# Kernel tuning notes

Hardware: AMD Instinct MI355X
Metric: run time of the kernel (lower is better)

The kernel has to match this reference:

```python
import jax, jax.numpy as jnp
import numpy as np

B, S, D, H, NL, V, E, DFF = 4, 512, 768, 12, 2, 32000, 8, 3072
CF = 1.25
HD = D // H


def setup_inputs() -> dict:
    key = jax.random.key(0)
    ks = jax.random.split(key, 12)
    r = lambda i, shape: jax.random.normal(ks[i], shape, jnp.float32) * 0.02
    return {
        "src": jax.random.randint(ks[0], (B, S), 0, V),
        "src_pad_mask": jnp.zeros((B, S), bool),
        "emb": r(1, (V, D)),
        "qkv_w": r(2, (NL, 3 * D, D)), "qkv_b": jnp.zeros((NL, 3 * D), jnp.float32),
        "out_w": r(3, (NL, D, D)), "out_b": jnp.zeros((NL, D), jnp.float32),
        "wr": r(4, (NL, D, E)),
        "w1": r(5, (NL, E, D, DFF)), "b1": jnp.zeros((NL, E, DFF), jnp.float32),
        "w2": r(6, (NL, E, DFF, D)), "b2": jnp.zeros((NL, E, D), jnp.float32),
        "ln1_g": jnp.ones((NL, D), jnp.float32), "ln1_b": jnp.zeros((NL, D), jnp.float32),
        "ln2_g": jnp.ones((NL, D), jnp.float32), "ln2_b": jnp.zeros((NL, D), jnp.float32),
        "lnf_g": jnp.ones((D,), jnp.float32), "lnf_b": jnp.zeros((D,), jnp.float32),
    }


def layernorm(x, g, b, eps=1e-5):
    mu = jnp.mean(x, -1, keepdims=True)
    var = jnp.mean((x - mu) ** 2, -1, keepdims=True)
    return (x - mu) * jax.lax.rsqrt(var + eps) * g + b


def pos_encoding():
    pos = jnp.arange(S, dtype=jnp.float32)[:, None]
    i = jnp.arange(0, D, 2, dtype=jnp.float32)
    ang = pos * jnp.exp(-(i / D) * jnp.log(jnp.float32(10000.0)))  # [S, D/2]
    pe = jnp.zeros((S, D), jnp.float32)
    pe = pe.at[:, 0::2].set(jnp.sin(ang)).at[:, 1::2].set(jnp.cos(ang))
    return pe


def mha(x, wqkv, bqkv, wo, bo, pad):
    qkv = x @ wqkv.T + bqkv
    q, k, v = jnp.split(qkv, 3, axis=-1)
    q = q.reshape(B, S, H, HD); k = k.reshape(B, S, H, HD); v = v.reshape(B, S, H, HD)
    sc = jnp.einsum('bqhd,bkhd->bhqk', q, k) * (1.0 / float(HD) ** 0.5)
    sc = jnp.where(pad[:, None, None, :], jnp.float32(-1e9), sc)
    at = jax.nn.softmax(sc, -1)
    o = jnp.einsum('bhqk,bkhd->bqhd', at, v).reshape(B, S, D)
    return o @ wo.T + bo


def switch_ffn(x, token_mask, wr, w1, b1, w2, b2):
    # Switch Transformer top-1 routing with capacity drop.
    T = B * S
    cap = int(CF * T / E)
    xf = x.reshape(T, D)
    vm = token_mask.reshape(T).astype(x.dtype)
    logits = xf @ wr                                   # [T, E]
    probs = jax.nn.softmax(logits, -1)
    idx = jnp.argmax(probs, -1)
    gate = jnp.take_along_axis(probs, idx[:, None], -1)[:, 0]
    oh = jax.nn.one_hot(idx, E, dtype=x.dtype) * vm[:, None]      # [T, E]
    pos = jnp.cumsum(oh, axis=0) * oh                  # 1-indexed position in expert
    keep = ((pos > 0) & (pos <= cap)).astype(x.dtype)
    disp = keep[:, :, None] * jax.nn.one_hot((pos - 1).astype(jnp.int32), cap, dtype=x.dtype)  # [T,E,C]
    comb = disp * gate[:, None, None]
    ein = jnp.einsum('tec,td->ecd', disp, xf)          # [E, C, D]
    hid = jax.nn.relu(jnp.einsum('ecd,edf->ecf', ein, w1) + b1[:, None, :])
    eo = jnp.einsum('ecf,efd->ecd', hid, w2) + b2[:, None, :]
    y = jnp.einsum('tec,ecd->td', comb, eo).reshape(B, S, D)
    denom = jnp.maximum(vm.sum(), 1.0)
    me = (probs * vm[:, None]).sum(0) / denom
    ce = oh.sum(0) / denom
    lb = jnp.float32(E) * jnp.sum(me * ce)
    z = jnp.sum((jax.nn.logsumexp(logits, -1) ** 2) * vm) / denom
    return y, lb, z


def forward(src, src_pad_mask, emb, qkv_w, qkv_b, out_w, out_b, wr, w1, b1, w2, b2,
            ln1_g, ln1_b, ln2_g, ln2_b, lnf_g, lnf_b):
    x = emb[src] * jnp.float32(float(D) ** 0.5) + pos_encoding()[None]
    token_mask = ~src_pad_mask
    lbs, zs = [], []
    for l in range(NL):
        xn = layernorm(x, ln1_g[l], ln1_b[l])
        x = x + mha(xn, qkv_w[l], qkv_b[l], out_w[l], out_b[l], src_pad_mask)
        xn = layernorm(x, ln2_g[l], ln2_b[l])
        y, lb, z = switch_ffn(xn, token_mask, wr[l], w1[l], b1[l], w2[l], b2[l])
        x = x + y
        lbs.append(lb); zs.append(z)
    x = layernorm(x, lnf_g, lnf_b)
    return x, jnp.stack(lbs).mean(), jnp.stack(zs).mean()


def reference(src, src_pad_mask, emb, qkv_w, qkv_b, out_w, out_b, wr, w1, b1, w2, b2,
              ln1_g, ln1_b, ln2_g, ln2_b, lnf_g, lnf_b):
    return forward(src, src_pad_mask, emb, qkv_w, qkv_b, out_w, out_b, wr, w1, b1, w2, b2,
                   ln1_g, ln1_b, ln2_g, ln2_b, lnf_g, lnf_b)
```

## Files before the change

kernel.cpp:

```cpp
#include <hip/hip_runtime.h>

#define BB 4
#define SS 512
#define DD 768
#define HH 12
#define NLAYER 2
#define EE 8
#define DFF 3072
#define TT 2048
#define CAP 320
#define HD 64

typedef unsigned short u16;
typedef long long ll;
typedef _Float16 f16x8 __attribute__((ext_vector_type(8)));
typedef float f32x4 __attribute__((ext_vector_type(4)));

union F16U { _Float16 h; u16 u; };

__device__ __forceinline__ void split2h(float v, u16& h0, u16& h1) {
    F16U c0; c0.h = (_Float16)v;
    float r = (v - (float)c0.h) * 4096.0f;
    F16U c1; c1.h = (_Float16)r;
    h0 = c0.u; h1 = c1.u;
}
__device__ __forceinline__ float rec2h(u16 a, u16 b) {
    F16U c0, c1; c0.u = a; c1.u = b;
    return (float)c0.h + (float)c1.h * (1.0f / 4096.0f);
}

#define MFMA16(a, b, c) __builtin_amdgcn_mfma_f32_16x16x32_f16(a, b, c, 0, 0, 0)

struct GemmP {
    const u16* A = nullptr; ll sAp = 0;
    const void* B = nullptr; ll sBp = 0;
    const float* bias = nullptr; ll biasStride = 0;
    void* C = nullptr; ll sCp = 0;
    int M = 0, N = 0, K = 0, lda = 0, ldb = 0, ldc = 0;
    int modA = 1; ll sA1 = 0, sA2 = 0;
    int modB = 1; ll sB1 = 0, sB2 = 0;
    int modC = 1; ll sC1 = 0, sC2 = 0;
    float alpha = 1.f;
    int flags = 0;
    int KS = 1; ll partStride = 0;
    int Jc = 1;
};

#define PADK 36

template<bool BTRANS, int NS>
__global__ __launch_bounds__(256) void gemm_kernel(GemmP p) {
    __shared__ u16 Al[NS][128][PADK];
    __shared__ u16 Bl[NS][128][PADK];
    const int tid = threadIdx.x;

    int bx, by, bz;
    {
        int gx = gridDim.x, gy = gridDim.y;
        int NBt = gx * gy * gridDim.z;
        int L = blockIdx.x + gx * (blockIdx.y + gy * blockIdx.z);
        int q = NBt >> 3, r = NBt & 7;
        int xcd = L & 7, wi = L >> 3;
        int c = (xcd < r) ? xcd * (q + 1) + wi : r * (q + 1) + (xcd - r) * q + wi;
        int Jc = p.Jc;
        int gxJ = gx * Jc;
        int sj = c / gxJ;
        int t = c - sj * gxJ;
        bx = t / Jc;
        int j = sj * Jc + (t - (t / Jc) * Jc);
        by = j % gy; bz = j / gy;
    }
    const int n0 = bx * 128, m0 = by * 128;
    const int slice = bz % p.KS;
    const int z = bz / p.KS;
    const int kslice = p.K / p.KS;
    const int k0 = slice * kslice;
    const int nkt = kslice >> 5;

    const u16* Ap = p.A + (ll)(z % p.modA) * p.sA1 + (ll)(z / p.modA) * p.sA2 + k0;
    const ll zB = (ll)(z % p.modB) * p.sB1 + (ll)(z / p.modB) * p.sB2;
    const ll zC = (ll)(z % p.modC) * p.sC1 + (ll)(z / p.modC) * p.sC2;
    const u16* Bpu = BTRANS ? ((const u16*)p.B + zB + k0) : nullptr;
    const float* Bpf = BTRANS ? nullptr : ((const float*)p.B + zB);

    const int lane = tid & 63, wid = tid >> 6;
    const int wm = (wid >> 1) * 64, wn = (wid & 1) * 64;
    const int ar = lane & 15, kg = (lane >> 4) * 8;

    f32x4 acc0[4][4] = {};
    f32x4 acc1[4][4] = {};

    uint4 ra[2 * NS];
    uint4 rb[2 * NS];
    float4 rbf4[4];

    auto loadA = [&](int kt) {
        #pragma unroll
        for (int s = 0; s < NS; ++s)
            #pragma unroll
            for (int h = 0; h < 2; ++h) {
                int c = tid + h * 256, row = c >> 2, q = c & 3;
                int gm = m0 + row;
                uint4 v = {0u, 0u, 0u, 0u};
                if (gm < p.M) v = *(const uint4*)(Ap + (ll)s * p.sAp + (size_t)gm * p.lda + kt * 32 + q * 8);
                ra[s * 2 + h] = v;
            }
    };
    auto storeA = [&]() {
        #pragma unroll
        for (int s = 0; s < NS; ++s)
            #pragma unroll
            for (int h = 0; h < 2; ++h) {
                int c = tid + h * 256, row = c >> 2, q = c & 3;
                *(uint4*)&Al[s][row][q * 8] = ra[s * 2 + h];
            }
    };
    auto loadB = [&](int kt) {
        if (BTRANS) {
            #pragma unroll
            for (int s = 0; s < NS; ++s)
                #pragma unroll
                for (int h = 0; h < 2; ++h) {
                    int c = tid + h * 256, row = c >> 2, q = c & 3;
                    int gn = n0 + row;
                    uint4 v = {0u, 0u, 0u, 0u};
                    if (gn < p.N) v = *(const uint4*)(Bpu + (ll)s * p.sBp + (size_t)gn * p.ldb + kt * 32 + q * 8);
                    rb[s * 2 + h] = v;
                }
        } else {
            #pragma unroll
            for (int it = 0; it < 4; ++it) {
                int kk = (tid >> 5) + it * 8;
                int gn = n0 + (tid & 31) * 4;
                float4 v = {0.f, 0.f, 0.f, 0.f};
                if (gn < p.N) v = *(const float4*)(Bpf + (size_t)(k0 + kt * 32 + kk) * p.ldb + gn);
                rbf4[it] = v;
            }
        }
    };
    auto storeB = [&]() {
        if (BTRANS) {
            #pragma unroll
            for (int s = 0; s < NS; ++s)
                #pragma unroll
                for (int h = 0; h < 2; ++h) {
                    int c = tid + h * 256, row = c >> 2, q = c & 3;
                    *(uint4*)&Bl[s][row][q * 8] = rb[s * 2 + h];
                }
        } else {
            int c4 = (tid & 31) * 4;
            #pragma unroll
            for (int it = 0; it < 4; ++it) {
                int kk = (tid >> 5) + it * 8;
                float vv[4] = {rbf4[it].x, rbf4[it].y, rbf4[it].z, rbf4[it].w};
                #pragma unroll
                for (int e = 0; e < 4; ++e) {
                    u16 h0, h1;
                    split2h(vv[e], h0, h1);
                    Bl[0][c4 + e][kk] = h0;
                    if (NS == 2) Bl[1][c4 + e][kk] = h1;
                }
            }
        }
    };

    loadA(0); loadB(0);
    for (int kt = 0; kt < nkt; ++kt) {
        storeA(); storeB();
        __syncthreads();
        if (kt + 1 < nkt) { loadA(kt + 1); loadB(kt + 1); }
        f16x8 b0r[4], b1r[4];
        #pragma unroll
        for (int j = 0; j < 4; ++j) {
            b0r[j] = *(const f16x8*)&Bl[0][wn + j * 16 + ar][kg];
            if (NS == 2) b1r[j] = *(const f16x8*)&Bl[1][wn + j * 16 + ar][kg];
        }
        #pragma unroll
        for (int i = 0; i < 4; ++i) {
            f16x8 a0 = *(const f16x8*)&Al[0][wm + i * 16 + ar][kg];
            f16x8 a1;
            if (NS == 2) a1 = *(const f16x8*)&Al[1][wm + i * 16 + ar][kg];
            #pragma unroll
            for (int j = 0; j < 4; ++j) {
                acc0[i][j] = MFMA16(a0, b0r[j], acc0[i][j]);
                if (NS == 2) {
                    acc1[i][j] = MFMA16(a0, b1r[j], acc1[i][j]);
                    acc1[i][j] = MFMA16(a1, b0r[j], acc1[i][j]);
                }
            }
        }
        __syncthreads();
    }

    const bool doPart = (p.flags & 16);
    float* Cpart = doPart ? ((float*)p.C + (ll)slice * p.partStride + zC) : nullptr;
    const float* biasp = (p.flags & 1) ? (p.bias + (ll)z * p.biasStride) : nullptr;
    u16* C0 = (!doPart && (p.flags & 8)) ? ((u16*)p.C + zC) : nullptr;
    u16* C1 = C0 ? (C0 + p.sCp) : nullptr;
    float* Cf = (!doPart && !(p.flags & 8)) ? ((float*)p.C + zC) : nullptr;
    #pragma unroll
    for (int i = 0; i < 4; ++i) {
        #pragma unroll
        for (int j = 0; j < 4; ++j) {
            int gc = n0 + wn + j * 16 + (lane & 15);
            if (gc >= p.N) continue;
            int gr0 = m0 + wm + i * 16 + (lane >> 4) * 4;
            #pragma unroll
            for (int r = 0; r < 4; ++r) {
                int gr = gr0 + r;
                if (gr >= p.M) continue;
                float v = acc0[i][j][r];
                if (NS == 2) v += acc1[i][j][r] * (1.0f / 4096.0f);
                v *= p.alpha;
                size_t off = (size_t)gr * p.ldc + gc;
                if (doPart) { Cpart[off] = v; continue; }
                if (p.flags & 1) v = __fadd_rn(v, biasp[gc]);
                if (p.flags & 2) v = fmaxf(v, 0.f);
                if (p.flags & 8) { u16 h0, h1; split2h(v, h0, h1); C0[off] = h0; C1[off] = h1; }
                else Cf[off] = v;
            }
        }
    }
}

__global__ __launch_bounds__(256) void flash_kernel(
    const u16* __restrict__ qkvp, ll sQp,
    const u16* __restrict__ vTp, ll sVp,
    const unsigned char* __restrict__ pad,
    u16* __restrict__ attnp, ll sOp) {
    __shared__ u16 KV[2][64][68];
    __shared__ u16 Pl[2][4][16][68];

    int L = blockIdx.x;
    int c = (L & 7) * 48 + (L >> 3);
    int bh = c >> 3, qt = c & 7;
    int b = bh / HH, h = bh % HH;
    int lane = threadIdx.x & 63, wv = threadIdx.x >> 6;
    int qbase = b * SS + qt * 64 + wv * 16;

    int spl = threadIdx.x >> 7;
    int srr = threadIdx.x & 127;
    int srow = srr >> 1, shalf = srr & 1;

    f16x8 qf[2][2];
    {
        const u16* qr = qkvp + (size_t)(qbase + (lane & 15)) * (3 * DD) + h * HD + (lane >> 4) * 8;
        #pragma unroll
        for (int kt2 = 0; kt2 < 2; ++kt2)
            #pragma unroll
            for (int pl = 0; pl < 2; ++pl)
                qf[kt2][pl] = *(const f16x8*)(qr + (ll)pl * sQp + kt2 * 32);
    }

    f32x4 S[32];
    #pragma unroll
    for (int kv = 0; kv < 8; ++kv) {
        const u16* gk = qkvp + (size_t)(b * SS + kv * 64 + srow) * (3 * DD) + DD + h * HD + (ll)spl * sQp;
        #pragma unroll
        for (int qq = 0; qq < 4; ++qq) {
            int off = shalf * 32 + qq * 8;
            *(uint4*)&KV[spl][srow][off] = *(const uint4*)(gk + off);
        }
        __syncthreads();
        #pragma unroll
        for (int nf = 0; nf < 4; ++nf) {
            f32x4 a0 = {}, a1 = {};
            #pragma unroll
            for (int kt2 = 0; kt2 < 2; ++kt2) {
                f16x8 b0 = *(const f16x8*)&KV[0][nf * 16 + (lane & 15)][kt2 * 32 + (lane >> 4) * 8];
                f16x8 b1 = *(const f16x8*)&KV[1][nf * 16 + (lane & 15)][kt2 * 32 + (lane >> 4) * 8];
                a0 = MFMA16(qf[kt2][0], b0, a0);
                a1 = MFMA16(qf[kt2][0], b1, a1);
                a1 = MFMA16(qf[kt2][1], b0, a1);
            }
            int col = kv * 64 + nf * 16 + (lane & 15);
            bool msk = pad[b * SS + col] != 0;
            #pragma unroll
            for (int r = 0; r < 4; ++r) {
                float v = (a0[r] + a1[r] * (1.0f / 4096.0f)) * 0.125f;
                S[kv * 4 + nf][r] = msk ? -1e9f : v;
            }
        }
        __syncthreads();
    }

    float mx[4] = {-1e30f, -1e30f, -1e30f, -1e30f}, sm[4] = {0.f, 0.f, 0.f, 0.f}, inv[4];
    #pragma unroll
    for (int f = 0; f < 32; ++f)
        #pragma unroll
        for (int r = 0; r < 4; ++r) mx[r] = fmaxf(mx[r], S[f][r]);
    #pragma unroll
    for (int r = 0; r < 4; ++r) {
        #pragma unroll
        for (int off = 1; off < 16; off <<= 1) mx[r] = fmaxf(mx[r], __shfl_xor(mx[r], off));
    }
    #pragma unroll
    for (int f = 0; f < 32; ++f)
        #pragma unroll
        for (int r = 0; r < 4; ++r) { float e = expf(S[f][r] - mx[r]); S[f][r] = e; sm[r] += e; }
    #pragma unroll
    for (int r = 0; r < 4; ++r) {
        #pragma unroll
        for (int off = 1; off < 16; off <<= 1) sm[r] += __shfl_xor(sm[r], off);
        inv[r] = 1.f / sm[r];
    }

    f32x4 p0[4] = {}, p1[4] = {};
    #pragma unroll
    for (int kv = 0; kv < 8; ++kv) {
        const u16* gv = vTp + (size_t)bh * HD * SS + (size_t)srow * SS + kv * 64 + (ll)spl * sVp;
        #pragma unroll
        for (int qq = 0; qq < 4; ++qq) {
            int off = shalf * 32 + qq * 8;
            *(uint4*)&KV[spl][srow][off] = *(const uint4*)(gv + off);
        }
        #pragma unroll
        for (int nf = 0; nf < 4; ++nf)
            #pragma unroll
            for (int r = 0; r < 4; ++r) {
                float v = S[kv * 4 + nf][r] * inv[r];
                u16 h0, h1; split2h(v, h0, h1);
                Pl[0][wv][(lane >> 4) * 4 + r][nf * 16 + (lane & 15)] = h0;
                Pl[1][wv][(lane >> 4) * 4 + r][nf * 16 + (lane & 15)] = h1;
            }
        __syncthreads();
        f16x8 pa[2][2];
        #pragma unroll
        for (int kt2 = 0; kt2 < 2; ++kt2)
            #pragma unroll
            for (int pl = 0; pl < 2; ++pl)
                pa[kt2][pl] = *(const f16x8*)&Pl[pl][wv][lane & 15][kt2 * 32 + (lane >> 4) * 8];
        #pragma unroll
        for (int df = 0; df < 4; ++df) {
            #pragma unroll
            for (int kt2 = 0; kt2 < 2; ++kt2) {
                f16x8 v0 = *(const f16x8*)&KV[0][df * 16 + (lane & 15)][kt2 * 32 + (lane >> 4) * 8];
                f16x8 v1 = *(const f16x8*)&KV[1][df * 16 + (lane & 15)][kt2 * 32 + (lane >> 4) * 8];
                p0[df] = MFMA16(pa[kt2][0], v0, p0[df]);
                p1[df] = MFMA16(pa[kt2][0], v1, p1[df]);
                p1[df] = MFMA16(pa[kt2][1], v0, p1[df]);
            }
        }
        __syncthreads();
    }

    #pragma unroll
    for (int df = 0; df < 4; ++df)
        #pragma unroll
        for (int r = 0; r < 4; ++r) {
            float v = p0[df][r] + p1[df][r] * (1.0f / 4096.0f);
            int row = qbase + (lane >> 4) * 4 + r;
            int col = h * HD + df * 16 + (lane & 15);
            u16 h0, h1; split2h(v, h0, h1);
            attnp[(size_t)row * DD + col] = h0;
            attnp[(size_t)row * DD + col + sOp] = h1;
        }
}

struct RedP {
    const float* part = nullptr; ll partStride = 0; int KS = 1;
    float* outf = nullptr;
    u16* o0 = nullptr; ll planeStride = 0;
    const float* bias = nullptr; ll biasStride = 0; ll batchElems = 1; int Nc = 1;
    const float* src = nullptr;
    ll total = 0; int mode = 0;
};
__global__ void reduce_kernel(RedP p) {
    ll e0 = ((ll)blockIdx.x * 256 + threadIdx.x) * 4;
    if (e0 >= p.total) return;
    float4 s = *(const float4*)(p.part + e0);
    for (int k = 1; k < p.KS; ++k) {
        float4 t = *(const float4*)(p.part + (ll)k * p.partStride + e0);
        s.x += t.x; s.y += t.y; s.z += t.z; s.w += t.w;
    }
    if (p.mode & 1) {
        ll b = e0 / p.batchElems;
        int d = (int)(e0 % p.Nc);
        float4 bv = *(const float4*)(p.bias + b * p.biasStride + d);
        s.x = __fadd_rn(s.x, bv.x); s.y = __fadd_rn(s.y, bv.y);
        s.z = __fadd_rn(s.z, bv.z); s.w = __fadd_rn(s.w, bv.w);
    }
    if (p.mode & 4) {
        float4 t = *(const float4*)(p.src + e0);
        s.x = __fadd_rn(s.x, t.x); s.y = __fadd_rn(s.y, t.y);
        s.z = __fadd_rn(s.z, t.z); s.w = __fadd_rn(s.w, t.w);
    }
    if (p.mode & 2) { s.x = fmaxf(s.x, 0.f); s.y = fmaxf(s.y, 0.f); s.z = fmaxf(s.z, 0.f); s.w = fmaxf(s.w, 0.f); }
    if (p.mode & 8) {
        u16 t0[4], t1[4];
        float vv[4] = {s.x, s.y, s.z, s.w};
        #pragma unroll
        for (int e = 0; e < 4; ++e) split2h(vv[e], t0[e], t1[e]);
        *(uint2*)(p.o0 + e0) = *(uint2*)t0;
        *(uint2*)(p.o0 + p.planeStride + e0) = *(uint2*)t1;
    } else {
        *(float4*)(p.outf + e0) = s;
    }
}

__global__ void wsplit_kernel(const float* __restrict__ w, u16* __restrict__ p0,
                              ll planeStride, ll total) {
    ll e0 = ((ll)blockIdx.x * 256 + threadIdx.x) * 4;
    if (e0 >= total) return;
    float4 v = *(const float4*)(w + e0);
    u16 t0[4], t1[4];
    float vv[4] = {v.x, v.y, v.z, v.w};
    #pragma unroll
    for (int e = 0; e < 4; ++e) split2h(vv[e], t0[e], t1[e]);
    *(uint2*)(p0 + e0) = *(uint2*)t0;
    *(uint2*)(p0 + planeStride + e0) = *(uint2*)t1;
}

__global__ void vtrans_kernel(const u16* __restrict__ qkvp, ll sQp,
                              u16* __restrict__ vTp, ll sVp) {
    __shared__ float t[32][33];
    int z = blockIdx.z;
    int b = z / HH, h = z % HH;
    int c0 = blockIdx.x * 32, r0 = blockIdx.y * 32;
    int tx = threadIdx.x, ty = threadIdx.y;
    const u16* in = qkvp + (size_t)(b * SS) * (3 * DD) + 2 * DD + h * HD;
    #pragma unroll
    for (int i = 0; i < 32; i += 8) {
        size_t o = (size_t)(r0 + ty + i) * (3 * DD) + c0 + tx;
        t[ty + i][tx] = rec2h(in[o], in[o + sQp]);
    }
    __syncthreads();
    u16* out = vTp + (size_t)z * HD * SS;
    #pragma unroll
    for (int i = 0; i < 32; i += 8) {
        size_t o = (size_t)(c0 + ty + i) * SS + r0 + tx;
        u16 h0, h1; split2h(t[tx][ty + i], h0, h1);
        out[o] = h0; out[o + sVp] = h1;
    }
}

__global__ void pe_kernel(float* __restrict__ pe) {
    int s = blockIdx.x, tid = threadIdx.x;
    const float lg = 9.210340371976184f;
    #pragma unroll
    for (int j = 0; j < 3; ++j) {
        int d = j * 256 + tid;
        int half = d >> 1;
        float fi = (float)(2 * half) / 768.0f;
        float arg = __fmul_rn(-fi, lg);
        float freq = (float)exp((double)arg);
        float ang = __fmul_rn((float)s, freq);
        double da = (double)ang;
        pe[(size_t)s * DD + d] = (d & 1) ? (float)cos(da) : (float)sin(da);
    }
}

__global__ void embed_kernel(const int* __restrict__ src, const float* __restrict__ emb,
                             const float* __restrict__ pe, float* __restrict__ x) {
    int t = blockIdx.x, tid = threadIdx.x;
    int s = t & (SS - 1);
    int tok = src[t];
    const float sq = 27.712812921102035f;
    #pragma unroll
    for (int j = 0; j < 3; ++j) {
        int d = j * 256 + tid;
        float e = emb[(size_t)tok * DD + d];
        x[(size_t)t * DD + d] = __fadd_rn(__fmul_rn(e, sq), pe[(size_t)s * DD + d]);
    }
}

__global__ void ln_kernel(const float* __restrict__ x, const float* __restrict__ g,
                          const float* __restrict__ b, float* __restrict__ outf,
                          u16* __restrict__ op, ll planeStride) {
    int t = blockIdx.x, tid = threadIdx.x;
    const float* xr = x + (size_t)t * DD;
    float v[3], s = 0.f, sq = 0.f;
    #pragma unroll
    for (int j = 0; j < 3; ++j) { v[j] = xr[tid + j * 256]; s += v[j]; sq += v[j] * v[j]; }
    #pragma unroll
    for (int off = 32; off; off >>= 1) { s += __shfl_xor(s, off); sq += __shfl_xor(sq, off); }
    __shared__ float rs[4], rq[4];
    int wid = tid >> 6;
    if ((tid & 63) == 0) { rs[wid] = s; rq[wid] = sq; }
    __syncthreads();
    s = rs[0] + rs[1] + rs[2] + rs[3];
    sq = rq[0] + rq[1] + rq[2] + rq[3];
    float mu = s / 768.0f;
    float var = sq / 768.0f - mu * mu;
    float rstd = rsqrtf(var + 1e-5f);
    #pragma unroll
    for (int j = 0; j < 3; ++j) {
        int d = tid + j * 256;
        float y = __fadd_rn(__fmul_rn(__fmul_rn(v[j] - mu, rstd), g[d]), b[d]);
        if (outf) outf[(size_t)t * DD + d] = y;
        size_t o = (size_t)t * DD + d;
        u16 h0, h1; split2h(y, h0, h1);
        op[o] = h0; op[o + planeStride] = h1;
    }
}

__global__ void router_kernel(const float* __restrict__ xn, const float* __restrict__ wr,
                              const unsigned char* __restrict__ pad,
                              float* __restrict__ probs, float* __restrict__ lsev,
                              float* __restrict__ gate, int* __restrict__ idx) {
    int t = blockIdx.x, lane = threadIdx.x;
    float a[8] = {0.f, 0.f, 0.f, 0.f, 0.f, 0.f, 0.f, 0.f};
    const float* xr = xn + (size_t)t * DD;
    for (int d = lane; d < DD; d += 64) {
        float xv = xr[d];
        const float* w = wr + (size_t)d * EE;
        #pragma unroll
        for (int e = 0; e < 8; ++e) a[e] += xv * w[e];
    }
    #pragma unroll
    for (int off = 32; off; off >>= 1)
        #pragma unroll
        for (int e = 0; e < 8; ++e) a[e] += __shfl_xor(a[e], off);
    if (lane == 0) {
        int vm = (pad[t] == 0);
        float mx = a[0]; int bi = 0;
        #pragma unroll
        for (int e = 1; e < 8; ++e) if (a[e] > mx) { mx = a[e]; bi = e; }
        float ex[8], sum = 0.f;
        #pragma unroll
        for (int e = 0; e < 8; ++e) { ex[e] = expf(a[e] - mx); sum += ex[e]; }
        float inv = 1.f / sum;
        #pragma unroll
        for (int e = 0; e < 8; ++e) probs[(size_t)t * EE + e] = vm ? ex[e] * inv : 0.f;
        lsev[t] = vm ? (mx + logf(sum)) : 0.f;
        gate[t] = ex[bi] * inv;
        idx[t] = vm ? bi : -1;
    }
}

__global__ void route_scan_kernel(const int* __restrict__ idx, const float* __restrict__ probs,
                                  const float* __restrict__ lsev, int* __restrict__ slot,
                                  int* __restrict__ tos, float* __restrict__ acc) {
    int lane = threadIdx.x;
    int base = lane * 32;
    int ev[32];
    int c[8] = {0, 0, 0, 0, 0, 0, 0, 0};
    #pragma unroll
    for (int i = 0; i < 32; ++i) {
        int e = idx[base + i];
        ev[i] = e;
        #pragma unroll
        for (int q = 0; q < 8; ++q) c[q] += (e == q);
    }
    int excl[8], tot[8];
    #pragma unroll
    for (int e = 0; e < 8; ++e) {
        int v = c[e];
        #pragma unroll
        for (int off = 1; off < 64; off <<= 1) {
            int n = __shfl_up(v, off);
            if (lane >= off) v += n;
        }
        excl[e] = v - c[e];
        tot[e] = __shfl(v, 63);
    }
    int r[8];
    #pragma unroll
    for (int e = 0; e < 8; ++e) r[e] = excl[e];
    #pragma unroll
    for (int i = 0; i < 32; ++i) {
        int t = base + i, e = ev[i], s = -1;
        if (e >= 0) {
            int pos = 0;
            #pragma unroll
            for (int q = 0; q < 8; ++q) if (e == q) { r[q]++; pos = r[q]; }
            if (pos <= CAP) { s = e * CAP + pos - 1; tos[s] = t; }
        }
        slot[t] = s;
    }
    float pa[8] = {0.f, 0.f, 0.f, 0.f, 0.f, 0.f, 0.f, 0.f};
    float l2 = 0.f, vld = 0.f;
    #pragma unroll
    for (int i = 0; i < 32; ++i) {
        int t = base + i;
        float lv = lsev[t];
        l2 += lv * lv;
        if (ev[i] >= 0) vld += 1.f;
        #pragma unroll
        for (int e = 0; e < 8; ++e) pa[e] += probs[(size_t)t * EE + e];
    }
    #pragma unroll
    for (int off = 32; off; off >>= 1) {
        #pragma unroll
        for (int e = 0; e < 8; ++e) pa[e] += __shfl_xor(pa[e], off);
        l2 += __shfl_xor(l2, off);
        vld += __shfl_xor(vld, off);
    }
    if (lane == 0) {
        float denom = fmaxf(vld, 1.f);
        float lb = 0.f;
        #pragma unroll
        for (int e = 0; e < 8; ++e) lb += (pa[e] / denom) * ((float)tot[e] / denom);
        lb *= 8.f;
        acc[0] += lb;
        acc[1] += l2 / denom;
    }
}

__global__ void gather_kernel(const int* __restrict__ tos, const u16* __restrict__ xnp,
                              ll sXp, u16* __restrict__ einp, ll sEp) {
    int s = blockIdx.x;
    int tid = threadIdx.x;
    if (tid >= 192) return;
    int pl = tid / 96, q = tid % 96;
    int t = tos[s];
    uint4 v = {0u, 0u, 0u, 0u};
    if (t >= 0) v = *(const uint4*)(xnp + (ll)pl * sXp + (size_t)t * DD + q * 8);
    *(uint4*)(einp + (ll)pl * sEp + (size_t)s * DD + q * 8) = v;
}

__global__ void combine_kernel(const int* __restrict__ slot, const float* __restrict__ gate,
                               const float* __restrict__ eo, float* __restrict__ x) {
    int t = blockIdx.x, tid = threadIdx.x;
    int s = slot[t];
    if (s < 0) return;
    float gv = gate[t];
    #pragma unroll
    for (int j = 0; j < 3; ++j) {
        int d = j * 256 + tid;
        size_t o = (size_t)t * DD + d;
        x[o] = __fadd_rn(x[o], __fmul_rn(gv, eo[(size_t)s * DD + d]));
    }
}

__global__ void finalize_kernel(const float* __restrict__ acc, float* __restrict__ out) {
    out[(size_t)TT * DD] = acc[0] * (1.f / NLAYER);
    out[(size_t)TT * DD + 1] = acc[1] * (1.f / NLAYER);
}

static inline void run_gemm(bool btrans, int ns, const GemmP& p, dim3 grid, hipStream_t s) {
    if (btrans) {
        gemm_kernel<true, 2><<<grid, 256, 0, s>>>(p);
    } else {
        if (ns == 2) gemm_kernel<false, 2><<<grid, 256, 0, s>>>(p);
        else gemm_kernel<false, 1><<<grid, 256, 0, s>>>(p);
    }
}
static inline void run_reduce(const RedP& r, hipStream_t s) {
    reduce_kernel<<<(int)((r.total / 4 + 255) / 256), 256, 0, s>>>(r);
}

extern "C" void kernel_launch(void* const* d_in, const int* in_sizes, int n_in,
                              void* d_out, int out_size, void* d_ws, size_t ws_size,
                              hipStream_t stream) {
    const int* src = (const int*)d_in[0];
    const unsigned char* pad = (const unsigned char*)d_in[1];
    const float* emb = (const float*)d_in[2];
    const float* qkv_w = (const float*)d_in[3];
    const float* qkv_b = (const float*)d_in[4];
    const float* out_w = (const float*)d_in[5];
    const float* out_b = (const float*)d_in[6];
    const float* wr = (const float*)d_in[7];
    const float* w1 = (const float*)d_in[8];
    const float* b1 = (const float*)d_in[9];
    const float* w2 = (const float*)d_in[10];
    const float* b2 = (const float*)d_in[11];
    const float* ln1_g = (const float*)d_in[12];
    const float* ln1_b = (const float*)d_in[13];
    const float* ln2_g = (const float*)d_in[14];
    const float* ln2_b = (const float*)d_in[15];
    const float* lnf_g = (const float*)d_in[16];
    const float* lnf_b = (const float*)d_in[17];

    char* w = (char*)d_ws;
    size_t off = 0;
    auto alloc = [&](size_t bytes) -> void* {
        void* p = w + off;
        off += (bytes + 255) & ~(size_t)255;
        return p;
    };
    float* x      = (float*)alloc((size_t)TT * DD * 4);
    float* xn     = (float*)alloc((size_t)TT * DD * 4);
    float* peT    = (float*)alloc((size_t)SS * DD * 4);
    u16*   xnp    = (u16*)  alloc((size_t)2 * TT * DD * 2);
    u16*   qkvp   = (u16*)  alloc((size_t)2 * TT * 3 * DD * 2);
    u16*   vTp    = (u16*)  alloc((size_t)2 * BB * HH * HD * SS * 2);
    u16*   attnp  = (u16*)  alloc((size_t)2 * TT * DD * 2);
    u16*   einp   = (u16*)  alloc((size_t)2 * EE * CAP * DD * 2);
    u16*   hidp   = (u16*)  alloc((size_t)2 * EE * CAP * DFF * 2);
    float* eo     = (float*)alloc((size_t)EE * CAP * DD * 4);
    char*  regB   = (char*) alloc((size_t)2 * EE * CAP * DFF * 4);
    u16*   qkvwp  = (u16*)  alloc((size_t)2 * NLAYER * 3 * DD * DD * 2);
    u16*   owp    = (u16*)  alloc((size_t)2 * NLAYER * DD * DD * 2);
    float* probs  = (float*)alloc((size_t)TT * EE * 4);
    float* lsev   = (float*)alloc((size_t)TT * 4);
    float* gate   = (float*)alloc((size_t)TT * 4);
    int*   idx    = (int*)  alloc((size_t)TT * 4);
    int*   slot   = (int*)  alloc((size_t)TT * 4);
    int*   tos    = (int*)  alloc((size_t)EE * CAP * 4);
    float* accb   = (float*)alloc(256);
    if (off > ws_size) return;

    float* qkvpart = (float*)regB;
    float* oppart  = (float*)regB;
    float* ffnpart = (float*)regB;

    hipMemsetAsync(accb, 0, 8, stream);
    pe_kernel<<<SS, 256, 0, stream>>>(peT);
    embed_kernel<<<TT, 256, 0, stream>>>(src, emb, peT, x);

    {
        ll tq = (ll)NLAYER * 3 * DD * DD;
        wsplit_kernel<<<(int)((tq / 4 + 255) / 256), 256, 0, stream>>>(qkv_w, qkvwp, tq, tq);
        ll to = (ll)NLAYER * DD * DD;
        wsplit_kernel<<<(int)((to / 4 + 255) / 256), 256, 0, stream>>>(out_w, owp, to, to);
    }

    for (int l = 0; l < NLAYER; ++l) {
        const int nsF = (l < NLAYER - 1) ? 2 : 1;
        ln_kernel<<<TT, 256, 0, stream>>>(x, ln1_g + l * DD, ln1_b + l * DD, nullptr, xnp, (ll)TT * DD);

        {
            GemmP p;
            p.A = xnp; p.sAp = (ll)TT * DD; p.lda = DD;
            p.B = qkvwp + (size_t)l * 3 * DD * DD; p.sBp = (ll)NLAYER * 3 * DD * DD; p.ldb = DD;
            p.C = qkvpart; p.ldc = 3 * DD;
            p.M = TT; p.N = 3 * DD; p.K = DD;
            p.flags = 16; p.KS = 2; p.partStride = (ll)TT * 3 * DD;
            p.Jc = 4;
            run_gemm(true, 2, p, dim3(18, 16, 2), stream);
        }
        {
            RedP r;
            r.part = qkvpart; r.partStride = (ll)TT * 3 * DD; r.KS = 2;
            r.o0 = qkvp; r.planeStride = (ll)TT * 3 * DD;
            r.bias = qkv_b + (size_t)l * 3 * DD; r.biasStride = 0; r.batchElems = (ll)TT * 3 * DD; r.Nc = 3 * DD;
            r.total = (ll)TT * 3 * DD; r.mode = 1 | 8;
            run_reduce(r, stream);
        }
        vtrans_kernel<<<dim3(HD / 32, SS / 32, BB * HH), dim3(32, 8), 0, stream>>>(
            qkvp, (ll)TT * 3 * DD, vTp, (ll)BB * HH * HD * SS);
        flash_kernel<<<BB * HH * 8, 256, 0, stream>>>(
            qkvp, (ll)TT * 3 * DD, vTp, (ll)BB * HH * HD * SS, pad, attnp, (ll)TT * DD);
        {
            GemmP p;
            p.A = attnp; p.sAp = (ll)TT * DD; p.lda = DD;
            p.B = owp + (size_t)l * DD * DD; p.sBp = (ll)NLAYER * DD * DD; p.ldb = DD;
            p.C = oppart; p.ldc = DD;
            p.M = TT; p.N = DD; p.K = DD;
            p.flags = 16; p.KS = 4; p.partStride = (ll)TT * DD;
            p.Jc = 8;
            run_gemm(true, 2, p, dim3(6, 16, 4), stream);
        }
        {
            RedP r;
            r.part = oppart; r.partStride = (ll)TT * DD; r.KS = 4;
            r.outf = x;
            r.bias = out_b + (size_t)l * DD; r.biasStride = 0; r.batchElems = (ll)TT * DD; r.Nc = DD;
            r.src = x;
            r.total = (ll)TT * DD; r.mode = 1 | 4;
            run_reduce(r, stream);
        }
        ln_kernel<<<TT, 256, 0, stream>>>(x, ln2_g + l * DD, ln2_b + l * DD, xn, xnp, (ll)TT * DD);
        router_kernel<<<TT, 64, 0, stream>>>(xn, wr + (size_t)l * DD * EE, pad, probs, lsev, gate, idx);
        hipMemsetAsync(tos, 0xFF, (size_t)EE * CAP * 4, stream);
        route_scan_kernel<<<1, 64, 0, stream>>>(idx, probs, lsev, slot, tos, accb);
        gather_kernel<<<EE * CAP, 256, 0, stream>>>(tos, xnp, (ll)TT * DD, einp, (ll)EE * CAP * DD);
        {
            GemmP p;
            p.A = einp; p.sAp = (ll)EE * CAP * DD; p.lda = DD;
            p.modA = EE; p.sA1 = (ll)CAP * DD;
            p.B = w1 + (size_t)l * EE * DD * DFF; p.ldb = DFF;
            p.modB = EE; p.sB1 = (ll)DD * DFF;
            p.C = ffnpart; p.ldc = DFF; p.modC = EE; p.sC1 = (ll)CAP * DFF;
            p.M = CAP; p.N = DFF; p.K = DD;
            p.flags = 16; p.KS = 2; p.partStride = (ll)EE * CAP * DFF;
            p.Jc = 6;
            run_gemm(false, nsF, p, dim3(24, 3, EE * 2), stream);
        }
        {
            RedP r;
            r.part = ffnpart; r.partStride = (ll)EE * CAP * DFF; r.KS = 2;
            r.o0 = hidp; r.planeStride = (ll)EE * CAP * DFF;
            r.bias = b1 + (size_t)l * EE * DFF; r.biasStride = DFF; r.batchElems = (ll)CAP * DFF; r.Nc = DFF;
            r.total = (ll)EE * CAP * DFF; r.mode = 1 | 2 | 8;
            run_reduce(r, stream);
        }
        {
            GemmP p;
            p.A = hidp; p.sAp = (ll)EE * CAP * DFF; p.lda = DFF;
            p.modA = EE; p.sA1 = (ll)CAP * DFF;
            p.B = w2 + (size_t)l * EE * DFF * DD; p.ldb = DD;
            p.modB = EE; p.sB1 = (ll)DFF * DD;
            p.C = ffnpart; p.ldc = DD; p.modC = EE; p.sC1 = (ll)CAP * DD;
            p.M = CAP; p.N = DD; p.K = DFF;
            p.flags = 16; p.KS = 4; p.partStride = (ll)EE * CAP * DD;
            p.Jc = 6;
            run_gemm(false, nsF, p, dim3(6, 3, EE * 4), stream);
        }
        {
            RedP r;
            r.part = ffnpart; r.partStride = (ll)EE * CAP * DD; r.KS = 4;
            r.outf = eo;
            r.bias = b2 + (size_t)l * EE * DD; r.biasStride = DD; r.batchElems = (ll)CAP * DD; r.Nc = DD;
            r.total = (ll)EE * CAP * DD; r.mode = 1;
            run_reduce(r, stream);
        }
        combine_kernel<<<TT, 256, 0, stream>>>(slot, gate, eo, x);
    }
    ln_kernel<<<TT, 256, 0, stream>>>(x, lnf_g, lnf_b, (float*)d_out, xnp, (ll)TT * DD);
    finalize_kernel<<<1, 1, 0, stream>>>(accb, (float*)d_out);
}
```

Measured before the change: 914.0 us.

## Fuse LN2 with router, pad shared tiles, vectorize fp32 B-tile LDS stores

Merges the second layernorm and the router into one kernel, which drops the fp32 xn buffer write/read and one launch per layer. The final layernorm no longer writes the unused fp16 split planes. LDS row padding changes from 36 to 40 halves in the GEMM and from 68 to 72 in the flash kernel, presumably to avoid bank conflicts and keep accesses aligned. The non-transposed fp32 B loader now has each thread load one column over several k values, so it can write 4 consecutive k as a uint2. The cost is scalar global loads instead of float4 loads.

Result: faster. 830.0 us (-9.2%).

```diff
diff --git a/kernel.cpp b/kernel.cpp
--- a/kernel.cpp
+++ b/kernel.cpp
@@ -46,7 +46,7 @@
     int Jc = 1;
 };
 
-#define PADK 36
+#define PADK 40
 
 template<bool BTRANS, int NS>
 __global__ __launch_bounds__(256) void gemm_kernel(GemmP p) {
@@ -92,7 +92,7 @@
 
     uint4 ra[2 * NS];
     uint4 rb[2 * NS];
-    float4 rbf4[4];
+    float rbf[16];
 
     auto loadA = [&](int kt) {
         #pragma unroll
@@ -129,13 +129,15 @@
                 }
         } else {
             #pragma unroll
-            for (int it = 0; it < 4; ++it) {
-                int kk = (tid >> 5) + it * 8;
-                int gn = n0 + (tid & 31) * 4;
-                float4 v = {0.f, 0.f, 0.f, 0.f};
-                if (gn < p.N) v = *(const float4*)(Bpf + (size_t)(k0 + kt * 32 + kk) * p.ldb + gn);
-                rbf4[it] = v;
-            }
+            for (int it = 0; it < 4; ++it)
+                #pragma unroll
+                for (int e = 0; e < 4; ++e) {
+                    int kk = (tid >> 7) * 16 + it * 4 + e;
+                    int gn = n0 + (tid & 127);
+                    float v = 0.f;
+                    if (gn < p.N) v = Bpf[(size_t)(k0 + kt * 32 + kk) * p.ldb + gn];
+                    rbf[it * 4 + e] = v;
+                }
         }
     };
     auto storeB = [&]() {
@@ -148,18 +150,15 @@
                     *(uint4*)&Bl[s][row][q * 8] = rb[s * 2 + h];
                 }
         } else {
-            int c4 = (tid & 31) * 4;
+            int col = tid & 127;
             #pragma unroll
             for (int it = 0; it < 4; ++it) {
-                int kk = (tid >> 5) + it * 8;
-                float vv[4] = {rbf4[it].x, rbf4[it].y, rbf4[it].z, rbf4[it].w};
+                int kq = (tid >> 7) * 16 + it * 4;
+                u16 t0[4], t1[4];
                 #pragma unroll
-                for (int e = 0; e < 4; ++e) {
-                    u16 h0, h1;
-                    split2h(vv[e], h0, h1);
-                    Bl[0][c4 + e][kk] = h0;
-                    if (NS == 2) Bl[1][c4 + e][kk] = h1;
-                }
+                for (int e = 0; e < 4; ++e) split2h(rbf[it * 4 + e], t0[e], t1[e]);
+                *(uint2*)&Bl[0][col][kq] = *(uint2*)t0;
+                if (NS == 2) *(uint2*)&Bl[1][col][kq] = *(uint2*)t1;
             }
         }
     };
@@ -228,8 +227,8 @@
     const u16* __restrict__ vTp, ll sVp,
     const unsigned char* __restrict__ pad,
     u16* __restrict__ attnp, ll sOp) {
-    __shared__ u16 KV[2][64][68];
-    __shared__ u16 Pl[2][4][16][68];
+    __shared__ u16 KV[2][64][72];
+    __shared__ u16 Pl[2][4][16][72];
 
     int L = blockIdx.x;
     int c = (L & 7) * 48 + (L >> 3);
@@ -488,30 +487,60 @@
         int d = tid + j * 256;
         float y = __fadd_rn(__fmul_rn(__fmul_rn(v[j] - mu, rstd), g[d]), b[d]);
         if (outf) outf[(size_t)t * DD + d] = y;
+        if (op) {
+            size_t o = (size_t)t * DD + d;
+            u16 h0, h1; split2h(y, h0, h1);
+            op[o] = h0; op[o + planeStride] = h1;
+        }
+    }
+}
+
+__global__ void ln2_router_kernel(const float* __restrict__ x, const float* __restrict__ g,
+                                  const float* __restrict__ b, const float* __restrict__ wr,
+                                  const unsigned char* __restrict__ pad,
+                                  u16* __restrict__ op, ll planeStride,
+                                  float* __restrict__ probs, float* __restrict__ lsev,
+                                  float* __restrict__ gate, int* __restrict__ idx) {
+    int t = blockIdx.x, tid = threadIdx.x;
+    const float* xr = x + (size_t)t * DD;
+    float v[3], s = 0.f, sq = 0.f;
+    #pragma unroll
+    for (int j = 0; j < 3; ++j) { v[j] = xr[tid + j * 256]; s += v[j]; sq += v[j] * v[j]; }
+    #pragma unroll
+    for (int off = 32; off; off >>= 1) { s += __shfl_xor(s, off); sq += __shfl_xor(sq, off); }
+    __shared__ float rs[4], rq[4];
+    __shared__ float ra[4][8];
+    int wid = tid >> 6;
+    if ((tid & 63) == 0) { rs[wid] = s; rq[wid] = sq; }
+    __syncthreads();
+    s = rs[0] + rs[1] + rs[2] + rs[3];
+    sq = rq[0] + rq[1] + rq[2] + rq[3];
+    float mu = s / 768.0f;
+    float var = sq / 768.0f - mu * mu;
+    float rstd = rsqrtf(var + 1e-5f);
+    float a[8] = {0.f, 0.f, 0.f, 0.f, 0.f, 0.f, 0.f, 0.f};
+    #pragma unroll
+    for (int j = 0; j < 3; ++j) {
+        int d = tid + j * 256;
+        float y = __fadd_rn(__fmul_rn(__fmul_rn(v[j] - mu, rstd), g[d]), b[d]);
         size_t o = (size_t)t * DD + d;
         u16 h0, h1; split2h(y, h0, h1);
         op[o] = h0; op[o + planeStride] = h1;
-    }
-}
-
-__global__ void router_kernel(const float* __restrict__ xn, const float* __restrict__ wr,
-                              const unsigned char* __restrict__ pad,
-                              float* __restrict__ probs, float* __restrict__ lsev,
-                              float* __restrict__ gate, int* __restrict__ idx) {
-    int t = blockIdx.x, lane = threadIdx.x;
-    float a[8] = {0.f, 0.f, 0.f, 0.f, 0.f, 0.f, 0.f, 0.f};
-    const float* xr = xn + (size_t)t * DD;
-    for (int d = lane; d < DD; d += 64) {
-        float xv = xr[d];
         const float* w = wr + (size_t)d * EE;
         #pragma unroll
-        for (int e = 0; e < 8; ++e) a[e] += xv * w[e];
+        for (int e = 0; e < 8; ++e) a[e] += y * w[e];
     }
     #pragma unroll
     for (int off = 32; off; off >>= 1)
         #pragma unroll
         for (int e = 0; e < 8; ++e) a[e] += __shfl_xor(a[e], off);
-    if (lane == 0) {
+    if ((tid & 63) == 0)
+        #pragma unroll
+        for (int e = 0; e < 8; ++e) ra[wid][e] = a[e];
+    __syncthreads();
+    if (tid == 0) {
+        #pragma unroll
+        for (int e = 0; e < 8; ++e) a[e] = ra[0][e] + ra[1][e] + ra[2][e] + ra[3][e];
         int vm = (pad[t] == 0);
         float mx = a[0]; int bi = 0;
         #pragma unroll
@@ -670,7 +699,6 @@
         return p;
     };
     float* x      = (float*)alloc((size_t)TT * DD * 4);
-    float* xn     = (float*)alloc((size_t)TT * DD * 4);
     float* peT    = (float*)alloc((size_t)SS * DD * 4);
     u16*   xnp    = (u16*)  alloc((size_t)2 * TT * DD * 2);
     u16*   qkvp   = (u16*)  alloc((size_t)2 * TT * 3 * DD * 2);
@@ -751,8 +779,9 @@
             r.total = (ll)TT * DD; r.mode = 1 | 4;
             run_reduce(r, stream);
         }
-        ln_kernel<<<TT, 256, 0, stream>>>(x, ln2_g + l * DD, ln2_b + l * DD, xn, xnp, (ll)TT * DD);
-        router_kernel<<<TT, 64, 0, stream>>>(xn, wr + (size_t)l * DD * EE, pad, probs, lsev, gate, idx);
+        ln2_router_kernel<<<TT, 256, 0, stream>>>(x, ln2_g + l * DD, ln2_b + l * DD,
+                                                  wr + (size_t)l * DD * EE, pad,
+                                                  xnp, (ll)TT * DD, probs, lsev, gate, idx);
         hipMemsetAsync(tos, 0xFF, (size_t)EE * CAP * 4, stream);
         route_scan_kernel<<<1, 64, 0, stream>>>(idx, probs, lsev, slot, tos, accb);
         gather_kernel<<<EE * CAP, 256, 0, stream>>>(tos, xnp, (ll)TT * DD, einp, (ll)EE * CAP * DD);
@@ -798,6 +827,6 @@
         }
         combine_kernel<<<TT, 256, 0, stream>>>(slot, gate, eo, x);
     }
-    ln_kernel<<<TT, 256, 0, stream>>>(x, lnf_g, lnf_b, (float*)d_out, xnp, (ll)TT * DD);
+    ln_kernel<<<TT, 256, 0, stream>>>(x, lnf_g, lnf_b, (float*)d_out, nullptr, 0);
     finalize_kernel<<<1, 1, 0, stream>>>(accb, (float*)d_out);
 }
```
